# Performance work log

Measured on AMD Instinct MI355X. Metric: run time of the kernel, lower is better.

The kernel has to match this reference:

```python
import jax, jax.numpy as jnp
import numpy as np

B, QL, L = 4, 1024, 2048          # batch, new query tokens, cache capacity
H, KVH, D = 16, 4, 128            # query heads, kv heads (GQA), head dim
G = H // KVH                      # query heads per kv head
SCALE = 1.0 / float(np.sqrt(D))
NEG = jnp.float32(-1e30)


def setup_inputs() -> dict:
    key = jax.random.key(0)
    ks = jax.random.split(key, 6)
    return {
        "q": jax.random.normal(ks[0], (B, QL, H * D), jnp.float32),
        "k": jax.random.normal(ks[1], (B, QL, KVH * D), jnp.float32),
        "v": jax.random.normal(ks[2], (B, QL, KVH * D), jnp.float32),
        "cache_k": jax.random.normal(ks[3], (B, KVH, L, D), jnp.float32),
        "cache_v": jax.random.normal(ks[4], (B, KVH, L, D), jnp.float32),
        "seq_lens": jax.random.randint(ks[5], (B,), 0, L - QL, jnp.int32),
    }


def reference(q, k, v, cache_k, cache_v, seq_lens):
    bs, ql, _ = q.shape
    # split heads; scale applied to q as in _jax_attn_func
    qh = (q.reshape(bs, ql, H, D) * SCALE).swapaxes(1, 2)   # [B,H,QL,D]
    kh = k.reshape(bs, ql, KVH, D)                           # [B,QL,KVH,D]
    vh = v.reshape(bs, ql, KVH, D)
    # write new tokens into the kv cache at per-sequence positions (ragged)
    pos = seq_lens[:, None] + jnp.arange(ql)                 # [B,QL]
    bidx = jnp.arange(bs)[:, None]                           # [B,1]
    new_ck = cache_k.at[bidx, :, pos].set(kh)                # [B,KVH,L,D]
    new_cv = cache_v.at[bidx, :, pos].set(vh)
    # GQA attention over the full cache with ragged-causal mask
    qg = qh.reshape(bs, KVH, G, ql, D)                       # [B,KVH,G,QL,D]
    scores = jnp.einsum('bkgqd,bkld->bkgql', qg, new_ck)     # [B,KVH,G,QL,L]
    limit = seq_lens[:, None, None, None, None] + jnp.arange(ql)[None, None, None, :, None]
    valid = jnp.arange(L)[None, None, None, None, :] <= limit
    scores = jnp.where(valid, scores, NEG)
    probs = jax.nn.softmax(scores, axis=-1)
    outg = jnp.einsum('bkgql,bkld->bkgqd', probs, new_cv)    # [B,KVH,G,QL,D]
    out = outg.reshape(bs, H, ql, D).swapaxes(1, 2).reshape(bs, ql, H * D)
    return (out, new_ck, new_cv)
```

## Files before the change

kernel.cpp:

```cpp
#include <hip/hip_runtime.h>
#include <hip/hip_bf16.h>
#include <stdint.h>

#define NB 4
#define NQL 1024
#define NL 2048
#define NH 16
#define NKVH 4
#define ND 128
#define KVBLK 64
#define QSCALE_LOG2E 0.1275174340213733f

typedef __bf16 bf16_t;
typedef __bf16 bf16x4 __attribute__((ext_vector_type(4)));
typedef __bf16 bf16x8 __attribute__((ext_vector_type(8)));
typedef float f32x4 __attribute__((ext_vector_type(4)));
typedef float f32x16 __attribute__((ext_vector_type(16)));
typedef uint32_t u32;
typedef unsigned short u16;

__device__ __forceinline__ void gload_lds16(const void* g, void* l) {
  __builtin_amdgcn_global_load_lds((const __attribute__((address_space(1))) void*)g,
                                   (__attribute__((address_space(3))) void*)l,
                                   16, 0, 0);
}

__device__ __forceinline__ u32 pack_bf16(float a, float b) {
  u32 ua = (u32)__builtin_bit_cast(u16, (bf16_t)a);
  u32 ub = (u32)__builtin_bit_cast(u16, (bf16_t)b);
  return ua | (ub << 16);
}

__global__ __launch_bounds__(256) void update_cache_kernel(
    const float* __restrict__ knew,
    const float* __restrict__ vnew,
    const float* __restrict__ cache_k,
    const float* __restrict__ cache_v,
    const int*   __restrict__ seq_lens,
    float* __restrict__ new_ck,
    float* __restrict__ new_cv,
    bf16_t* __restrict__ kb)
{
  const int n4 = NB * NKVH * NL * ND / 4;
  for (int i = blockIdx.x * blockDim.x + threadIdx.x; i < 2 * n4;
       i += gridDim.x * blockDim.x) {
    const int which = i >= n4;
    const int j   = which ? i - n4 : i;
    const int d4  = j & 31;
    const int l   = (j >> 5) & (NL - 1);
    const int kvh = (j >> 16) & (NKVH - 1);
    const int b   = j >> 18;
    const int s   = seq_lens[b];
    float4 val;
    if (l >= s && l < s + NQL) {
      const float* nsrc = which ? vnew : knew;
      val = *(const float4*)(nsrc + (((size_t)(b * NQL + (l - s))) * NKVH + kvh) * ND + d4 * 4);
    } else {
      const float* csrc = which ? cache_v : cache_k;
      val = *(const float4*)(csrc + (((size_t)(b * NKVH + kvh)) * NL + l) * ND + d4 * 4);
    }
    const size_t coff = (((size_t)(b * NKVH + kvh)) * NL + l) * ND + d4 * 4;
    float* dst = which ? new_cv : new_ck;
    *(float4*)(dst + coff) = val;
    if (!which) {
      bf16x4 kv;
      kv[0] = (bf16_t)val.x; kv[1] = (bf16_t)val.y;
      kv[2] = (bf16_t)val.z; kv[3] = (bf16_t)val.w;
      *(bf16x4*)(kb + coff) = kv;
    }
  }
}

__global__ __launch_bounds__(256) void transpose_v_kernel(
    const float* __restrict__ new_cv, bf16_t* __restrict__ vt)
{
  __shared__ float T[64][129];
  const int tid = threadIdx.x;
  const int bid = blockIdx.x;
  const int lt  = bid & 31;
  const int kvh = (bid >> 5) & (NKVH - 1);
  const int b   = bid >> 7;
  const int l0  = lt * 64;

  const float* src = new_cv + (((size_t)(b * NKVH + kvh)) * NL + l0) * ND;
  #pragma unroll
  for (int j = 0; j < 8; ++j) {
    const int i   = tid + j * 256;
    const int row = i >> 5, c4 = i & 31;
    float4 v = *(const float4*)(src + row * ND + c4 * 4);
    T[row][c4 * 4 + 0] = v.x; T[row][c4 * 4 + 1] = v.y;
    T[row][c4 * 4 + 2] = v.z; T[row][c4 * 4 + 3] = v.w;
  }
  __syncthreads();
  bf16_t* dst = vt + ((size_t)(b * NKVH + kvh)) * ND * NL;
  #pragma unroll
  for (int j = 0; j < 4; ++j) {
    const int c = tid + j * 256;
    const int d = c >> 3, l8 = c & 7;
    bf16x8 o;
    #pragma unroll
    for (int e = 0; e < 8; ++e) o[e] = (bf16_t)T[l8 * 8 + e][d];
    *(bf16x8*)(dst + (size_t)d * NL + l0 + l8 * 8) = o;
  }
}

#define STAGE_K(buf, tt) do {                                                \
    const int l0s = (tt) * KVBLK;                                            \
    _Pragma("unroll")                                                        \
    for (int j = 0; j < 4; ++j) {                                            \
      const int ck = tid + j * 256;                                          \
      const int kr = ck >> 4, kc2 = (ck & 15) ^ (kr & 7);                    \
      gload_lds16(kbb + (size_t)(l0s + kr) * ND + kc2 * 8,                   \
                  &Kl[buf][(wave * 64 + j * 256) * 8]);                      \
    }                                                                        \
  } while (0)

#define STAGE_V(buf, tt) do {                                                \
    const int l0s = (tt) * KVBLK;                                            \
    _Pragma("unroll")                                                        \
    for (int j = 0; j < 4; ++j) {                                            \
      const int ck = tid + j * 256;                                          \
      const int vr = ck >> 3, vc2 = (ck & 7) ^ (vr & 7);                     \
      gload_lds16(vtb + (size_t)vr * NL + (l0s + vc2 * 8),                   \
                  &Vl[buf][(wave * 64 + j * 256) * 8]);                      \
    }                                                                        \
  } while (0)

#define QKT(SB, KBI) do {                                                    \
    _Pragma("unroll")                                                        \
    for (int sl = 0; sl < 2; ++sl) {                                         \
      f32x16 acc = (f32x16)(0.f);                                            \
      const int krow = sl * 32 + l5;                                         \
      _Pragma("unroll")                                                      \
      for (int kc = 0; kc < 8; ++kc) {                                       \
        bf16x8 kf = *(const bf16x8*)                                         \
            &Kl[KBI][krow * ND + (((kc * 2 + hi5) ^ (l5 & 7)) * 8)];         \
        acc = __builtin_amdgcn_mfma_f32_32x32x16_bf16(kf, qf[kc], acc, 0, 0, 0); \
      }                                                                      \
      SB[sl] = acc;                                                          \
    }                                                                        \
  } while (0)

#define SOFTPV(SB, VBI, L0) do {                                             \
    if ((L0) + 63 > s + qw) {                                                \
      const int lim = s + q - (L0);                                          \
      _Pragma("unroll")                                                      \
      for (int sl = 0; sl < 2; ++sl)                                         \
        _Pragma("unroll")                                                    \
        for (int rr = 0; rr < 16; ++rr) {                                    \
          const int ll = sl * 32 + (rr & 3) + 8 * (rr >> 2) + 4 * hi5;       \
          if (ll > lim) SB[sl][rr] = -1e30f;                                 \
        }                                                                    \
    }                                                                        \
    float pmax = SB[0][0];                                                   \
    _Pragma("unroll")                                                        \
    for (int sl = 0; sl < 2; ++sl)                                           \
      _Pragma("unroll")                                                      \
      for (int rr = 0; rr < 16; ++rr) pmax = fmaxf(pmax, SB[sl][rr]);        \
    pmax = fmaxf(pmax, __shfl_xor(pmax, 32, 64));                            \
    if (!__all(pmax - mreg <= 8.f)) {                                        \
      const float mnew  = fmaxf(mreg, pmax);                                 \
      const float alpha = exp2f(mreg - mnew);                                \
      mreg = mnew;                                                           \
      lreg *= alpha;                                                         \
      _Pragma("unroll")                                                      \
      for (int i = 0; i < 4; ++i) oacc[i] *= alpha;                          \
    }                                                                        \
    float tsum = 0.f;                                                        \
    _Pragma("unroll")                                                        \
    for (int sl = 0; sl < 2; ++sl)                                           \
      _Pragma("unroll")                                                      \
      for (int rr = 0; rr < 16; ++rr) {                                      \
        const float p = exp2f(SB[sl][rr] - mreg);                            \
        SB[sl][rr] = p;                                                      \
        tsum += p;                                                           \
      }                                                                      \
    lreg += tsum + __shfl_xor(tsum, 32, 64);                                 \
    u32 pk[2][4][2];                                                         \
    _Pragma("unroll")                                                        \
    for (int sl = 0; sl < 2; ++sl)                                           \
      _Pragma("unroll")                                                      \
      for (int m = 0; m < 4; ++m) {                                          \
        pk[sl][m][0] = pack_bf16(SB[sl][m * 4 + 0], SB[sl][m * 4 + 1]);      \
        pk[sl][m][1] = pack_bf16(SB[sl][m * 4 + 2], SB[sl][m * 4 + 3]);      \
      }                                                                      \
    bf16x8 pb[4];                                                            \
    _Pragma("unroll")                                                        \
    for (int c = 0; c < 4; ++c) {                                            \
      const int slp = c >> 1;                                                \
      const u32 k0 = hi5 ? pk[slp][(2 * c + 1) & 3][0] : pk[slp][(2 * c) & 3][0]; \
      const u32 k1 = hi5 ? pk[slp][(2 * c + 1) & 3][1] : pk[slp][(2 * c) & 3][1]; \
      const u32 s0 = hi5 ? pk[slp][(2 * c) & 3][0] : pk[slp][(2 * c + 1) & 3][0]; \
      const u32 s1 = hi5 ? pk[slp][(2 * c) & 3][1] : pk[slp][(2 * c + 1) & 3][1]; \
      const u32 r0 = (u32)__shfl_xor((int)s0, 32, 64);                       \
      const u32 r1 = (u32)__shfl_xor((int)s1, 32, 64);                       \
      union { u32 w[4]; bf16x8 v; } u;                                       \
      u.w[0] = hi5 ? r0 : k0;                                                \
      u.w[1] = hi5 ? r1 : k1;                                                \
      u.w[2] = hi5 ? k0 : r0;                                                \
      u.w[3] = hi5 ? k1 : r1;                                                \
      pb[c] = u.v;                                                           \
    }                                                                        \
    _Pragma("unroll")                                                        \
    for (int ds = 0; ds < 4; ++ds) {                                         \
      const int vrow = ds * 32 + l5;                                         \
      _Pragma("unroll")                                                      \
      for (int c = 0; c < 4; ++c) {                                          \
        bf16x8 va = *(const bf16x8*)                                         \
            &Vl[VBI][vrow * KVBLK + (((c * 2 + hi5) ^ (l5 & 7)) * 8)];       \
        oacc[ds] = __builtin_amdgcn_mfma_f32_32x32x16_bf16(va, pb[c], oacc[ds], 0, 0, 0); \
      }                                                                      \
    }                                                                        \
  } while (0)

__global__ __launch_bounds__(256, 2) void attn_kernel(
    const float* __restrict__ qin, const bf16_t* __restrict__ kb,
    const bf16_t* __restrict__ vt, const int* __restrict__ seq_lens,
    float* __restrict__ out)
{
  __shared__ bf16_t Kl[2][KVBLK * ND];
  __shared__ bf16_t Vl[2][ND * KVBLK];

  const int tid  = threadIdx.x;
  const int wave = tid >> 6, lane = tid & 63;
  const int l5   = lane & 31;
  const int hi5  = lane >> 5;

  const int bid  = blockIdx.x;
  const int half = bid >> 8, r = bid & 255;
  const int b    = r >> 6;
  const int h    = (r >> 2) & (NH - 1);
  const int qt   = half ? (7 - ((r & 3) << 1)) : ((r & 3) << 1);
  const int kvh  = h >> 2;
  const int s    = seq_lens[b];
  const int qw   = qt * 128 + wave * 32;
  const int q    = qw + l5;

  const bf16_t* kbb = kb + ((size_t)(b * NKVH + kvh)) * NL * ND;
  const bf16_t* vtb = vt + ((size_t)(b * NKVH + kvh)) * ND * NL;

  bf16x8 qf[8];
  {
    const float* qb = qin + ((size_t)((b * NQL + q) * NH + h)) * ND;
    #pragma unroll
    for (int kc = 0; kc < 8; ++kc) {
      float4 x0 = *(const float4*)(qb + kc * 16 + hi5 * 8);
      float4 x1 = *(const float4*)(qb + kc * 16 + hi5 * 8 + 4);
      bf16x8 f;
      f[0] = (bf16_t)(x0.x * QSCALE_LOG2E); f[1] = (bf16_t)(x0.y * QSCALE_LOG2E);
      f[2] = (bf16_t)(x0.z * QSCALE_LOG2E); f[3] = (bf16_t)(x0.w * QSCALE_LOG2E);
      f[4] = (bf16_t)(x1.x * QSCALE_LOG2E); f[5] = (bf16_t)(x1.y * QSCALE_LOG2E);
      f[6] = (bf16_t)(x1.z * QSCALE_LOG2E); f[7] = (bf16_t)(x1.w * QSCALE_LOG2E);
      qf[kc] = f;
    }
  }

  f32x16 oacc[4];
  #pragma unroll
  for (int i = 0; i < 4; ++i) oacc[i] = (f32x16)(0.f);
  float mreg = -1e30f, lreg = 0.f;

  const int ntiles = (s + qt * 128 + 128 + KVBLK - 1) / KVBLK;

  STAGE_K(0, 0);
  STAGE_V(0, 0);
  STAGE_K(1, 1);
  __syncthreads();

  f32x16 sA[2], sB[2];
  QKT(sA, 0);

  for (int t = 0; ; t += 2) {
    __syncthreads();
    if (t + 2 < ntiles) STAGE_K(0, t + 2);
    if (t + 1 < ntiles) STAGE_V(1, t + 1);
    const bool gB = (t + 1 < ntiles) && ((t + 1) * KVBLK <= s + qw + 31);
    if (gB) QKT(sB, 1);
    if (t * KVBLK <= s + qw + 31) SOFTPV(sA, 0, t * KVBLK);
    if (t + 1 >= ntiles) break;

    __syncthreads();
    if (t + 3 < ntiles) STAGE_K(1, t + 3);
    if (t + 2 < ntiles) STAGE_V(0, t + 2);
    const bool gA = (t + 2 < ntiles) && ((t + 2) * KVBLK <= s + qw + 31);
    if (gA) QKT(sA, 0);
    if ((t + 1) * KVBLK <= s + qw + 31) SOFTPV(sB, 1, (t + 1) * KVBLK);
    if (t + 2 >= ntiles) break;
  }

  const float linv = 1.0f / lreg;
  float* ob = out + ((size_t)((b * NQL + q) * NH + h)) * ND;
  #pragma unroll
  for (int ds = 0; ds < 4; ++ds)
    #pragma unroll
    for (int rq = 0; rq < 4; ++rq) {
      float4 v;
      v.x = oacc[ds][rq * 4 + 0] * linv;
      v.y = oacc[ds][rq * 4 + 1] * linv;
      v.z = oacc[ds][rq * 4 + 2] * linv;
      v.w = oacc[ds][rq * 4 + 3] * linv;
      *(float4*)(ob + ds * 32 + rq * 8 + hi5 * 4) = v;
    }
}

extern "C" void kernel_launch(void* const* d_in, const int* in_sizes, int n_in,
                              void* d_out, int out_size, void* d_ws, size_t ws_size,
                              hipStream_t stream)
{
  const float* q        = (const float*)d_in[0];
  const float* k        = (const float*)d_in[1];
  const float* v        = (const float*)d_in[2];
  const float* cache_k  = (const float*)d_in[3];
  const float* cache_v  = (const float*)d_in[4];
  const int*   seq_lens = (const int*)d_in[5];

  float* out    = (float*)d_out;
  float* new_ck = out + (size_t)NB * NQL * NH * ND;
  float* new_cv = new_ck + (size_t)NB * NKVH * NL * ND;

  bf16_t* kb = (bf16_t*)d_ws;
  bf16_t* vt = kb + (size_t)NB * NKVH * NL * ND;

  hipLaunchKernelGGL(update_cache_kernel, dim3(2048), dim3(256), 0, stream,
                     k, v, cache_k, cache_v, seq_lens, new_ck, new_cv, kb);
  hipLaunchKernelGGL(transpose_v_kernel, dim3(NB * NKVH * (NL / 64)), dim3(256), 0, stream,
                     new_cv, vt);
  hipLaunchKernelGGL(attn_kernel, dim3(512), dim3(256), 0, stream,
                     q, kb, vt, seq_lens, out);
}
```

Before: 110.2 us.

## Switch attention to 16x16x32 MFMA with smaller query and KV tiles

Reworks the attention kernel to use 16x16x32 bf16 MFMA instead of 32x32x16. Each wave now handles 16 query rows, KV tiles shrink to 32 rows, and the grid grows from 512 to 1024 blocks with occupancy raised to 4 blocks per CU. The P-matrix relayout now uses shuffles suited to the 16x16 fragment layout, and the causal-load-balancing block ordering is dropped. The aim is more parallelism and finer causal skipping, at the cost of more synchronisation per KV element, less data reuse per tile, and more shuffle overhead.

Measured after the change: 131.9 us. +19.7%, slower.

```diff
diff --git a/kernel.cpp b/kernel.cpp
--- a/kernel.cpp
+++ b/kernel.cpp
@@ -8,14 +8,13 @@
 #define NH 16
 #define NKVH 4
 #define ND 128
-#define KVBLK 64
+#define KVBLK 32
 #define QSCALE_LOG2E 0.1275174340213733f
 
 typedef __bf16 bf16_t;
 typedef __bf16 bf16x4 __attribute__((ext_vector_type(4)));
 typedef __bf16 bf16x8 __attribute__((ext_vector_type(8)));
 typedef float f32x4 __attribute__((ext_vector_type(4)));
-typedef float f32x16 __attribute__((ext_vector_type(16)));
 typedef uint32_t u32;
 typedef unsigned short u16;
 
@@ -107,7 +106,7 @@
 #define STAGE_K(buf, tt) do {                                                \
     const int l0s = (tt) * KVBLK;                                            \
     _Pragma("unroll")                                                        \
-    for (int j = 0; j < 4; ++j) {                                            \
+    for (int j = 0; j < 2; ++j) {                                            \
       const int ck = tid + j * 256;                                          \
       const int kr = ck >> 4, kc2 = (ck & 15) ^ (kr & 7);                    \
       gload_lds16(kbb + (size_t)(l0s + kr) * ND + kc2 * 8,                   \
@@ -118,9 +117,9 @@
 #define STAGE_V(buf, tt) do {                                                \
     const int l0s = (tt) * KVBLK;                                            \
     _Pragma("unroll")                                                        \
-    for (int j = 0; j < 4; ++j) {                                            \
+    for (int j = 0; j < 2; ++j) {                                            \
       const int ck = tid + j * 256;                                          \
-      const int vr = ck >> 3, vc2 = (ck & 7) ^ (vr & 7);                     \
+      const int vr = ck >> 2, vc2 = (ck & 3) ^ (vr & 3);                     \
       gload_lds16(vtb + (size_t)vr * NL + (l0s + vc2 * 8),                   \
                   &Vl[buf][(wave * 64 + j * 256) * 8]);                      \
     }                                                                        \
@@ -129,91 +128,72 @@
 #define QKT(SB, KBI) do {                                                    \
     _Pragma("unroll")                                                        \
     for (int sl = 0; sl < 2; ++sl) {                                         \
-      f32x16 acc = (f32x16)(0.f);                                            \
-      const int krow = sl * 32 + l5;                                         \
+      f32x4 acc = (f32x4){0.f, 0.f, 0.f, 0.f};                               \
       _Pragma("unroll")                                                      \
-      for (int kc = 0; kc < 8; ++kc) {                                       \
+      for (int kc = 0; kc < 4; ++kc) {                                       \
         bf16x8 kf = *(const bf16x8*)                                         \
-            &Kl[KBI][krow * ND + (((kc * 2 + hi5) ^ (l5 & 7)) * 8)];         \
-        acc = __builtin_amdgcn_mfma_f32_32x32x16_bf16(kf, qf[kc], acc, 0, 0, 0); \
+            &Kl[KBI][((sl * 16 + llo) * 16 + ((kc * 4 + lhi) ^ (llo & 7))) * 8]; \
+        acc = __builtin_amdgcn_mfma_f32_16x16x32_bf16(kf, qf[kc], acc, 0, 0, 0); \
       }                                                                      \
       SB[sl] = acc;                                                          \
     }                                                                        \
   } while (0)
 
 #define SOFTPV(SB, VBI, L0) do {                                             \
-    if ((L0) + 63 > s + qw) {                                                \
+    if ((L0) + 31 > s + qw) {                                                \
       const int lim = s + q - (L0);                                          \
       _Pragma("unroll")                                                      \
       for (int sl = 0; sl < 2; ++sl)                                         \
         _Pragma("unroll")                                                    \
-        for (int rr = 0; rr < 16; ++rr) {                                    \
-          const int ll = sl * 32 + (rr & 3) + 8 * (rr >> 2) + 4 * hi5;       \
-          if (ll > lim) SB[sl][rr] = -1e30f;                                 \
-        }                                                                    \
-    }                                                                        \
-    float pmax = SB[0][0];                                                   \
-    _Pragma("unroll")                                                        \
-    for (int sl = 0; sl < 2; ++sl)                                           \
-      _Pragma("unroll")                                                      \
-      for (int rr = 0; rr < 16; ++rr) pmax = fmaxf(pmax, SB[sl][rr]);        \
-    pmax = fmaxf(pmax, __shfl_xor(pmax, 32, 64));                            \
-    if (!__all(pmax - mreg <= 8.f)) {                                        \
-      const float mnew  = fmaxf(mreg, pmax);                                 \
+        for (int rr = 0; rr < 4; ++rr)                                       \
+          if (sl * 16 + lhi * 4 + rr > lim) SB[sl][rr] = -1e30f;             \
+    }                                                                        \
+    float pm = fmaxf(fmaxf(fmaxf(SB[0][0], SB[0][1]), fmaxf(SB[0][2], SB[0][3])), \
+                     fmaxf(fmaxf(SB[1][0], SB[1][1]), fmaxf(SB[1][2], SB[1][3]))); \
+    pm = fmaxf(pm, __shfl_xor(pm, 16, 64));                                  \
+    pm = fmaxf(pm, __shfl_xor(pm, 32, 64));                                  \
+    if (!__all(pm - mreg <= 8.f)) {                                          \
+      const float mnew  = fmaxf(mreg, pm);                                   \
       const float alpha = exp2f(mreg - mnew);                                \
       mreg = mnew;                                                           \
       lreg *= alpha;                                                         \
       _Pragma("unroll")                                                      \
-      for (int i = 0; i < 4; ++i) oacc[i] *= alpha;                          \
-    }                                                                        \
-    float tsum = 0.f;                                                        \
+      for (int i = 0; i < 8; ++i) oacc[i] *= alpha;                          \
+    }                                                                        \
+    const float p0 = exp2f(SB[0][0] - mreg), p1 = exp2f(SB[0][1] - mreg);    \
+    const float p2 = exp2f(SB[0][2] - mreg), p3 = exp2f(SB[0][3] - mreg);    \
+    const float p4 = exp2f(SB[1][0] - mreg), p5 = exp2f(SB[1][1] - mreg);    \
+    const float p6 = exp2f(SB[1][2] - mreg), p7 = exp2f(SB[1][3] - mreg);    \
+    float ts = ((p0 + p1) + (p2 + p3)) + ((p4 + p5) + (p6 + p7));            \
+    ts += __shfl_xor(ts, 16, 64);                                            \
+    ts += __shfl_xor(ts, 32, 64);                                            \
+    lreg += ts;                                                              \
+    const u32 pk00 = pack_bf16(p0, p1), pk01 = pack_bf16(p2, p3);            \
+    const u32 pk10 = pack_bf16(p4, p5), pk11 = pack_bf16(p6, p7);            \
+    const int src0 = ((lhi & 1) << 5) + llo;                                 \
+    const int src1 = src0 + 16;                                              \
+    const u32 a00 = (u32)__shfl((int)pk00, src0, 64);                        \
+    const u32 a01 = (u32)__shfl((int)pk01, src0, 64);                        \
+    const u32 a02 = (u32)__shfl((int)pk00, src1, 64);                        \
+    const u32 a03 = (u32)__shfl((int)pk01, src1, 64);                        \
+    const u32 a10 = (u32)__shfl((int)pk10, src0, 64);                        \
+    const u32 a11 = (u32)__shfl((int)pk11, src0, 64);                        \
+    const u32 a12 = (u32)__shfl((int)pk10, src1, 64);                        \
+    const u32 a13 = (u32)__shfl((int)pk11, src1, 64);                        \
+    union { u32 w[4]; bf16x8 v; } uu;                                        \
+    uu.w[0] = (lhi < 2) ? a00 : a10;                                         \
+    uu.w[1] = (lhi < 2) ? a01 : a11;                                         \
+    uu.w[2] = (lhi < 2) ? a02 : a12;                                         \
+    uu.w[3] = (lhi < 2) ? a03 : a13;                                         \
     _Pragma("unroll")                                                        \
-    for (int sl = 0; sl < 2; ++sl)                                           \
-      _Pragma("unroll")                                                      \
-      for (int rr = 0; rr < 16; ++rr) {                                      \
-        const float p = exp2f(SB[sl][rr] - mreg);                            \
-        SB[sl][rr] = p;                                                      \
-        tsum += p;                                                           \
-      }                                                                      \
-    lreg += tsum + __shfl_xor(tsum, 32, 64);                                 \
-    u32 pk[2][4][2];                                                         \
-    _Pragma("unroll")                                                        \
-    for (int sl = 0; sl < 2; ++sl)                                           \
-      _Pragma("unroll")                                                      \
-      for (int m = 0; m < 4; ++m) {                                          \
-        pk[sl][m][0] = pack_bf16(SB[sl][m * 4 + 0], SB[sl][m * 4 + 1]);      \
-        pk[sl][m][1] = pack_bf16(SB[sl][m * 4 + 2], SB[sl][m * 4 + 3]);      \
-      }                                                                      \
-    bf16x8 pb[4];                                                            \
-    _Pragma("unroll")                                                        \
-    for (int c = 0; c < 4; ++c) {                                            \
-      const int slp = c >> 1;                                                \
-      const u32 k0 = hi5 ? pk[slp][(2 * c + 1) & 3][0] : pk[slp][(2 * c) & 3][0]; \
-      const u32 k1 = hi5 ? pk[slp][(2 * c + 1) & 3][1] : pk[slp][(2 * c) & 3][1]; \
-      const u32 s0 = hi5 ? pk[slp][(2 * c) & 3][0] : pk[slp][(2 * c + 1) & 3][0]; \
-      const u32 s1 = hi5 ? pk[slp][(2 * c) & 3][1] : pk[slp][(2 * c + 1) & 3][1]; \
-      const u32 r0 = (u32)__shfl_xor((int)s0, 32, 64);                       \
-      const u32 r1 = (u32)__shfl_xor((int)s1, 32, 64);                       \
-      union { u32 w[4]; bf16x8 v; } u;                                       \
-      u.w[0] = hi5 ? r0 : k0;                                                \
-      u.w[1] = hi5 ? r1 : k1;                                                \
-      u.w[2] = hi5 ? k0 : r0;                                                \
-      u.w[3] = hi5 ? k1 : r1;                                                \
-      pb[c] = u.v;                                                           \
-    }                                                                        \
-    _Pragma("unroll")                                                        \
-    for (int ds = 0; ds < 4; ++ds) {                                         \
-      const int vrow = ds * 32 + l5;                                         \
-      _Pragma("unroll")                                                      \
-      for (int c = 0; c < 4; ++c) {                                          \
-        bf16x8 va = *(const bf16x8*)                                         \
-            &Vl[VBI][vrow * KVBLK + (((c * 2 + hi5) ^ (l5 & 7)) * 8)];       \
-        oacc[ds] = __builtin_amdgcn_mfma_f32_32x32x16_bf16(va, pb[c], oacc[ds], 0, 0, 0); \
-      }                                                                      \
+    for (int dsb = 0; dsb < 8; ++dsb) {                                      \
+      bf16x8 va = *(const bf16x8*)                                           \
+          &Vl[VBI][((dsb * 16 + llo) * 4 + (lhi ^ (llo & 3))) * 8];          \
+      oacc[dsb] = __builtin_amdgcn_mfma_f32_16x16x32_bf16(va, uu.v, oacc[dsb], 0, 0, 0); \
     }                                                                        \
   } while (0)
 
-__global__ __launch_bounds__(256, 2) void attn_kernel(
+__global__ __launch_bounds__(256, 4) void attn_kernel(
     const float* __restrict__ qin, const bf16_t* __restrict__ kb,
     const bf16_t* __restrict__ vt, const int* __restrict__ seq_lens,
     float* __restrict__ out)
@@ -223,29 +203,29 @@
 
   const int tid  = threadIdx.x;
   const int wave = tid >> 6, lane = tid & 63;
-  const int l5   = lane & 31;
-  const int hi5  = lane >> 5;
-
-  const int bid  = blockIdx.x;
-  const int half = bid >> 8, r = bid & 255;
-  const int b    = r >> 6;
-  const int h    = (r >> 2) & (NH - 1);
-  const int qt   = half ? (7 - ((r & 3) << 1)) : ((r & 3) << 1);
-  const int kvh  = h >> 2;
-  const int s    = seq_lens[b];
-  const int qw   = qt * 128 + wave * 32;
-  const int q    = qw + l5;
+  const int llo  = lane & 15;
+  const int lhi  = lane >> 4;
+
+  const int bid = blockIdx.x;
+  const int b   = bid >> 8;
+  const int r   = bid & 255;
+  const int h   = r >> 4;
+  const int qt  = r & 15;
+  const int kvh = h >> 2;
+  const int s   = seq_lens[b];
+  const int qw  = qt * 64 + wave * 16;
+  const int q   = qw + llo;
 
   const bf16_t* kbb = kb + ((size_t)(b * NKVH + kvh)) * NL * ND;
   const bf16_t* vtb = vt + ((size_t)(b * NKVH + kvh)) * ND * NL;
 
-  bf16x8 qf[8];
+  bf16x8 qf[4];
   {
     const float* qb = qin + ((size_t)((b * NQL + q) * NH + h)) * ND;
     #pragma unroll
-    for (int kc = 0; kc < 8; ++kc) {
-      float4 x0 = *(const float4*)(qb + kc * 16 + hi5 * 8);
-      float4 x1 = *(const float4*)(qb + kc * 16 + hi5 * 8 + 4);
+    for (int kc = 0; kc < 4; ++kc) {
+      float4 x0 = *(const float4*)(qb + kc * 32 + lhi * 8);
+      float4 x1 = *(const float4*)(qb + kc * 32 + lhi * 8 + 4);
       bf16x8 f;
       f[0] = (bf16_t)(x0.x * QSCALE_LOG2E); f[1] = (bf16_t)(x0.y * QSCALE_LOG2E);
       f[2] = (bf16_t)(x0.z * QSCALE_LOG2E); f[3] = (bf16_t)(x0.w * QSCALE_LOG2E);
@@ -255,52 +235,50 @@
     }
   }
 
-  f32x16 oacc[4];
+  f32x4 oacc[8];
   #pragma unroll
-  for (int i = 0; i < 4; ++i) oacc[i] = (f32x16)(0.f);
+  for (int i = 0; i < 8; ++i) oacc[i] = (f32x4){0.f, 0.f, 0.f, 0.f};
   float mreg = -1e30f, lreg = 0.f;
 
-  const int ntiles = (s + qt * 128 + 128 + KVBLK - 1) / KVBLK;
+  const int ntiles = (s + qt * 64 + 64 + KVBLK - 1) / KVBLK;
 
   STAGE_K(0, 0);
   STAGE_V(0, 0);
   STAGE_K(1, 1);
   __syncthreads();
 
-  f32x16 sA[2], sB[2];
+  f32x4 sA[2], sB[2];
   QKT(sA, 0);
 
   for (int t = 0; ; t += 2) {
     __syncthreads();
     if (t + 2 < ntiles) STAGE_K(0, t + 2);
     if (t + 1 < ntiles) STAGE_V(1, t + 1);
-    const bool gB = (t + 1 < ntiles) && ((t + 1) * KVBLK <= s + qw + 31);
+    const bool gB = (t + 1 < ntiles) && ((t + 1) * KVBLK <= s + qw + 15);
     if (gB) QKT(sB, 1);
-    if (t * KVBLK <= s + qw + 31) SOFTPV(sA, 0, t * KVBLK);
+    if (t * KVBLK <= s + qw + 15) SOFTPV(sA, 0, t * KVBLK);
     if (t + 1 >= ntiles) break;
 
     __syncthreads();
     if (t + 3 < ntiles) STAGE_K(1, t + 3);
     if (t + 2 < ntiles) STAGE_V(0, t + 2);
-    const bool gA = (t + 2 < ntiles) && ((t + 2) * KVBLK <= s + qw + 31);
+    const bool gA = (t + 2 < ntiles) && ((t + 2) * KVBLK <= s + qw + 15);
     if (gA) QKT(sA, 0);
-    if ((t + 1) * KVBLK <= s + qw + 31) SOFTPV(sB, 1, (t + 1) * KVBLK);
+    if ((t + 1) * KVBLK <= s + qw + 15) SOFTPV(sB, 1, (t + 1) * KVBLK);
     if (t + 2 >= ntiles) break;
   }
 
   const float linv = 1.0f / lreg;
   float* ob = out + ((size_t)((b * NQL + q) * NH + h)) * ND;
   #pragma unroll
-  for (int ds = 0; ds < 4; ++ds)
-    #pragma unroll
-    for (int rq = 0; rq < 4; ++rq) {
-      float4 v;
-      v.x = oacc[ds][rq * 4 + 0] * linv;
-      v.y = oacc[ds][rq * 4 + 1] * linv;
-      v.z = oacc[ds][rq * 4 + 2] * linv;
-      v.w = oacc[ds][rq * 4 + 3] * linv;
-      *(float4*)(ob + ds * 32 + rq * 8 + hi5 * 4) = v;
-    }
+  for (int dsb = 0; dsb < 8; ++dsb) {
+    float4 v;
+    v.x = oacc[dsb][0] * linv;
+    v.y = oacc[dsb][1] * linv;
+    v.z = oacc[dsb][2] * linv;
+    v.w = oacc[dsb][3] * linv;
+    *(float4*)(ob + dsb * 16 + lhi * 4) = v;
+  }
 }
 
 extern "C" void kernel_launch(void* const* d_in, const int* in_sizes, int n_in,
@@ -325,6 +303,6 @@
                      k, v, cache_k, cache_v, seq_lens, new_ck, new_cv, kb);
   hipLaunchKernelGGL(transpose_v_kernel, dim3(NB * NKVH * (NL / 64)), dim3(256), 0, stream,
                      new_cv, vt);
-  hipLaunchKernelGGL(attn_kernel, dim3(512), dim3(256), 0, stream,
+  hipLaunchKernelGGL(attn_kernel, dim3(NB * NH * (NQL / 64)), dim3(256), 0, stream,
                      q, kb, vt, seq_lens, out);
 }
```

## Split KV range across two blocks with combine kernel and smaller KV tile

Applied to the files above, without the earlier changes.

Adds a split-KV (flash-decoding style) scheme: each (batch, kv head, q tile) is split into two KV ranges. Each range writes bf16 partial outputs plus running max and sum, and a new combine kernel merges them into the final output. The KV tile shrinks from 64 to 32 rows with a new V swizzle, and launch bounds rise to 4 blocks per SM to raise occupancy. The goal is more parallelism and better load balance across the causal triangle. The cost is an extra kernel launch, more global traffic for partials, and bf16 rounding of the partial accumulators.

New measurement: 262.7 us. 138% more time.

```diff
diff --git a/kernel.cpp b/kernel.cpp
--- a/kernel.cpp
+++ b/kernel.cpp
@@ -8,7 +8,8 @@
 #define NH 16
 #define NKVH 4
 #define ND 128
-#define KVBLK 64
+#define KVBLK 32
+#define NROWS (NB * NH * NQL)
 #define QSCALE_LOG2E 0.1275174340213733f
 
 typedef __bf16 bf16_t;
@@ -107,7 +108,7 @@
 #define STAGE_K(buf, tt) do {                                                \
     const int l0s = (tt) * KVBLK;                                            \
     _Pragma("unroll")                                                        \
-    for (int j = 0; j < 4; ++j) {                                            \
+    for (int j = 0; j < 2; ++j) {                                            \
       const int ck = tid + j * 256;                                          \
       const int kr = ck >> 4, kc2 = (ck & 15) ^ (kr & 7);                    \
       gload_lds16(kbb + (size_t)(l0s + kr) * ND + kc2 * 8,                   \
@@ -118,105 +119,93 @@
 #define STAGE_V(buf, tt) do {                                                \
     const int l0s = (tt) * KVBLK;                                            \
     _Pragma("unroll")                                                        \
-    for (int j = 0; j < 4; ++j) {                                            \
+    for (int j = 0; j < 2; ++j) {                                            \
       const int ck = tid + j * 256;                                          \
-      const int vr = ck >> 3, vc2 = (ck & 7) ^ (vr & 7);                     \
+      const int vr = ck >> 2, vc2 = (ck & 3) ^ ((vr ^ (vr >> 2)) & 3);       \
       gload_lds16(vtb + (size_t)vr * NL + (l0s + vc2 * 8),                   \
                   &Vl[buf][(wave * 64 + j * 256) * 8]);                      \
     }                                                                        \
   } while (0)
 
 #define QKT(SB, KBI) do {                                                    \
-    _Pragma("unroll")                                                        \
-    for (int sl = 0; sl < 2; ++sl) {                                         \
-      f32x16 acc = (f32x16)(0.f);                                            \
-      const int krow = sl * 32 + l5;                                         \
-      _Pragma("unroll")                                                      \
-      for (int kc = 0; kc < 8; ++kc) {                                       \
-        bf16x8 kf = *(const bf16x8*)                                         \
-            &Kl[KBI][krow * ND + (((kc * 2 + hi5) ^ (l5 & 7)) * 8)];         \
-        acc = __builtin_amdgcn_mfma_f32_32x32x16_bf16(kf, qf[kc], acc, 0, 0, 0); \
-      }                                                                      \
-      SB[sl] = acc;                                                          \
-    }                                                                        \
+    f32x16 acc = (f32x16)(0.f);                                              \
+    _Pragma("unroll")                                                        \
+    for (int kc = 0; kc < 8; ++kc) {                                         \
+      bf16x8 kf = *(const bf16x8*)                                           \
+          &Kl[KBI][(l5 * 16 + ((kc * 2 + hi5) ^ (l5 & 7))) * 8];             \
+      acc = __builtin_amdgcn_mfma_f32_32x32x16_bf16(kf, qf[kc], acc, 0, 0, 0); \
+    }                                                                        \
+    SB = acc;                                                                \
   } while (0)
 
 #define SOFTPV(SB, VBI, L0) do {                                             \
-    if ((L0) + 63 > s + qw) {                                                \
+    if ((L0) + 31 > s + qw) {                                                \
       const int lim = s + q - (L0);                                          \
       _Pragma("unroll")                                                      \
-      for (int sl = 0; sl < 2; ++sl)                                         \
-        _Pragma("unroll")                                                    \
-        for (int rr = 0; rr < 16; ++rr) {                                    \
-          const int ll = sl * 32 + (rr & 3) + 8 * (rr >> 2) + 4 * hi5;       \
-          if (ll > lim) SB[sl][rr] = -1e30f;                                 \
-        }                                                                    \
-    }                                                                        \
-    float pmax = SB[0][0];                                                   \
-    _Pragma("unroll")                                                        \
-    for (int sl = 0; sl < 2; ++sl)                                           \
-      _Pragma("unroll")                                                      \
-      for (int rr = 0; rr < 16; ++rr) pmax = fmaxf(pmax, SB[sl][rr]);        \
-    pmax = fmaxf(pmax, __shfl_xor(pmax, 32, 64));                            \
-    if (!__all(pmax - mreg <= 8.f)) {                                        \
-      const float mnew  = fmaxf(mreg, pmax);                                 \
+      for (int rr = 0; rr < 16; ++rr) {                                      \
+        const int ll = (rr & 3) + 8 * (rr >> 2) + 4 * hi5;                   \
+        if (ll > lim) SB[rr] = -1e30f;                                       \
+      }                                                                      \
+    }                                                                        \
+    float pm = SB[0];                                                        \
+    _Pragma("unroll")                                                        \
+    for (int rr = 1; rr < 16; ++rr) pm = fmaxf(pm, SB[rr]);                  \
+    pm = fmaxf(pm, __shfl_xor(pm, 32, 64));                                  \
+    if (!__all(pm - mreg <= 8.f)) {                                          \
+      const float mnew  = fmaxf(mreg, pm);                                   \
       const float alpha = exp2f(mreg - mnew);                                \
       mreg = mnew;                                                           \
       lreg *= alpha;                                                         \
       _Pragma("unroll")                                                      \
       for (int i = 0; i < 4; ++i) oacc[i] *= alpha;                          \
     }                                                                        \
-    float tsum = 0.f;                                                        \
-    _Pragma("unroll")                                                        \
-    for (int sl = 0; sl < 2; ++sl)                                           \
-      _Pragma("unroll")                                                      \
-      for (int rr = 0; rr < 16; ++rr) {                                      \
-        const float p = exp2f(SB[sl][rr] - mreg);                            \
-        SB[sl][rr] = p;                                                      \
-        tsum += p;                                                           \
-      }                                                                      \
-    lreg += tsum + __shfl_xor(tsum, 32, 64);                                 \
-    u32 pk[2][4][2];                                                         \
-    _Pragma("unroll")                                                        \
-    for (int sl = 0; sl < 2; ++sl)                                           \
-      _Pragma("unroll")                                                      \
-      for (int m = 0; m < 4; ++m) {                                          \
-        pk[sl][m][0] = pack_bf16(SB[sl][m * 4 + 0], SB[sl][m * 4 + 1]);      \
-        pk[sl][m][1] = pack_bf16(SB[sl][m * 4 + 2], SB[sl][m * 4 + 3]);      \
-      }                                                                      \
-    bf16x8 pb[4];                                                            \
-    _Pragma("unroll")                                                        \
-    for (int c = 0; c < 4; ++c) {                                            \
-      const int slp = c >> 1;                                                \
-      const u32 k0 = hi5 ? pk[slp][(2 * c + 1) & 3][0] : pk[slp][(2 * c) & 3][0]; \
-      const u32 k1 = hi5 ? pk[slp][(2 * c + 1) & 3][1] : pk[slp][(2 * c) & 3][1]; \
-      const u32 s0 = hi5 ? pk[slp][(2 * c) & 3][0] : pk[slp][(2 * c + 1) & 3][0]; \
-      const u32 s1 = hi5 ? pk[slp][(2 * c) & 3][1] : pk[slp][(2 * c + 1) & 3][1]; \
-      const u32 r0 = (u32)__shfl_xor((int)s0, 32, 64);                       \
-      const u32 r1 = (u32)__shfl_xor((int)s1, 32, 64);                       \
-      union { u32 w[4]; bf16x8 v; } u;                                       \
-      u.w[0] = hi5 ? r0 : k0;                                                \
-      u.w[1] = hi5 ? r1 : k1;                                                \
-      u.w[2] = hi5 ? k0 : r0;                                                \
-      u.w[3] = hi5 ? k1 : r1;                                                \
-      pb[c] = u.v;                                                           \
+    float ts = 0.f;                                                          \
+    _Pragma("unroll")                                                        \
+    for (int rr = 0; rr < 16; ++rr) {                                        \
+      const float p = exp2f(SB[rr] - mreg);                                  \
+      SB[rr] = p;                                                            \
+      ts += p;                                                               \
+    }                                                                        \
+    lreg += ts + __shfl_xor(ts, 32, 64);                                     \
+    u32 pk[4][2];                                                            \
+    _Pragma("unroll")                                                        \
+    for (int m = 0; m < 4; ++m) {                                            \
+      pk[m][0] = pack_bf16(SB[m * 4 + 0], SB[m * 4 + 1]);                    \
+      pk[m][1] = pack_bf16(SB[m * 4 + 2], SB[m * 4 + 3]);                    \
+    }                                                                        \
+    bf16x8 pb[2];                                                            \
+    _Pragma("unroll")                                                        \
+    for (int c = 0; c < 2; ++c) {                                            \
+      const u32 own0 = hi5 ? pk[c * 2 + 1][0] : pk[c * 2][0];                \
+      const u32 own1 = hi5 ? pk[c * 2 + 1][1] : pk[c * 2][1];                \
+      const u32 snd0 = hi5 ? pk[c * 2][0] : pk[c * 2 + 1][0];                \
+      const u32 snd1 = hi5 ? pk[c * 2][1] : pk[c * 2 + 1][1];                \
+      const u32 r0 = (u32)__shfl_xor((int)snd0, 32, 64);                     \
+      const u32 r1 = (u32)__shfl_xor((int)snd1, 32, 64);                     \
+      union { u32 w[4]; bf16x8 v; } uu;                                      \
+      uu.w[0] = hi5 ? r0 : own0;                                             \
+      uu.w[1] = hi5 ? r1 : own1;                                             \
+      uu.w[2] = hi5 ? own0 : r0;                                             \
+      uu.w[3] = hi5 ? own1 : r1;                                             \
+      pb[c] = uu.v;                                                          \
     }                                                                        \
     _Pragma("unroll")                                                        \
     for (int ds = 0; ds < 4; ++ds) {                                         \
       const int vrow = ds * 32 + l5;                                         \
       _Pragma("unroll")                                                      \
-      for (int c = 0; c < 4; ++c) {                                          \
+      for (int c = 0; c < 2; ++c) {                                          \
         bf16x8 va = *(const bf16x8*)                                         \
-            &Vl[VBI][vrow * KVBLK + (((c * 2 + hi5) ^ (l5 & 7)) * 8)];       \
+            &Vl[VBI][(vrow * 4 + ((c * 2 + hi5) ^ ((l5 ^ (l5 >> 2)) & 3))) * 8]; \
         oacc[ds] = __builtin_amdgcn_mfma_f32_32x32x16_bf16(va, pb[c], oacc[ds], 0, 0, 0); \
       }                                                                      \
     }                                                                        \
   } while (0)
 
-__global__ __launch_bounds__(256, 2) void attn_kernel(
+__global__ __launch_bounds__(256, 4) void attn_kernel(
     const float* __restrict__ qin, const bf16_t* __restrict__ kb,
     const bf16_t* __restrict__ vt, const int* __restrict__ seq_lens,
-    float* __restrict__ out)
+    float* __restrict__ out, bf16_t* __restrict__ opart,
+    float2* __restrict__ ml, int nspl)
 {
   __shared__ bf16_t Kl[2][KVBLK * ND];
   __shared__ bf16_t Vl[2][ND * KVBLK];
@@ -226,18 +215,21 @@
   const int l5   = lane & 31;
   const int hi5  = lane >> 5;
 
-  const int bid  = blockIdx.x;
-  const int half = bid >> 8, r = bid & 255;
-  const int b    = r >> 6;
-  const int h    = (r >> 2) & (NH - 1);
-  const int qt   = half ? (7 - ((r & 3) << 1)) : ((r & 3) << 1);
-  const int kvh  = h >> 2;
-  const int s    = seq_lens[b];
-  const int qw   = qt * 128 + wave * 32;
-  const int q    = qw + l5;
-
-  const bf16_t* kbb = kb + ((size_t)(b * NKVH + kvh)) * NL * ND;
-  const bf16_t* vtb = vt + ((size_t)(b * NKVH + kvh)) * ND * NL;
+  const int bid = blockIdx.x;
+  const int qt  = bid & 7;
+  const int hh  = (bid >> 3) & 3;
+  const int g   = bid >> 5;
+  const int sp  = g - (g / nspl) * nspl;
+  const int bk  = g / nspl;
+  const int kvh = bk & (NKVH - 1);
+  const int b   = bk >> 2;
+  const int h   = kvh * 4 + hh;
+  const int s   = seq_lens[b];
+  const int qw  = qt * 128 + wave * 32;
+  const int q   = qw + l5;
+
+  const bf16_t* kbb = kb + ((size_t)bk) * NL * ND;
+  const bf16_t* vtb = vt + ((size_t)bk) * ND * NL;
 
   bf16x8 qf[8];
   {
@@ -260,47 +252,90 @@
   for (int i = 0; i < 4; ++i) oacc[i] = (f32x16)(0.f);
   float mreg = -1e30f, lreg = 0.f;
 
-  const int ntiles = (s + qt * 128 + 128 + KVBLK - 1) / KVBLK;
-
-  STAGE_K(0, 0);
-  STAGE_V(0, 0);
-  STAGE_K(1, 1);
+  const int nt   = (s + qt * 128 + 128 + KVBLK - 1) / KVBLK;
+  const int half = (nt + nspl - 1) / nspl;
+  const int t0   = sp * half;
+  const int t1   = (sp + 1 == nspl) ? nt : (t0 + half);
+  const int vlim = s + qw + 31;
+
+  STAGE_K(0, t0);
+  STAGE_V(0, t0);
+  STAGE_K(1, t0 + 1);
   __syncthreads();
 
-  f32x16 sA[2], sB[2];
+  f32x16 sA, sB;
   QKT(sA, 0);
 
-  for (int t = 0; ; t += 2) {
+  for (int t = t0; ; t += 2) {
     __syncthreads();
-    if (t + 2 < ntiles) STAGE_K(0, t + 2);
-    if (t + 1 < ntiles) STAGE_V(1, t + 1);
-    const bool gB = (t + 1 < ntiles) && ((t + 1) * KVBLK <= s + qw + 31);
+    if (t + 2 < t1) STAGE_K(0, t + 2);
+    if (t + 1 < t1) STAGE_V(1, t + 1);
+    const bool gB = (t + 1 < t1) && ((t + 1) * KVBLK <= vlim);
     if (gB) QKT(sB, 1);
-    if (t * KVBLK <= s + qw + 31) SOFTPV(sA, 0, t * KVBLK);
-    if (t + 1 >= ntiles) break;
+    if (t * KVBLK <= vlim) SOFTPV(sA, 0, t * KVBLK);
+    if (t + 1 >= t1) break;
 
     __syncthreads();
-    if (t + 3 < ntiles) STAGE_K(1, t + 3);
-    if (t + 2 < ntiles) STAGE_V(0, t + 2);
-    const bool gA = (t + 2 < ntiles) && ((t + 2) * KVBLK <= s + qw + 31);
+    if (t + 3 < t1) STAGE_K(1, t + 3);
+    if (t + 2 < t1) STAGE_V(0, t + 2);
+    const bool gA = (t + 2 < t1) && ((t + 2) * KVBLK <= vlim);
     if (gA) QKT(sA, 0);
-    if ((t + 1) * KVBLK <= s + qw + 31) SOFTPV(sB, 1, (t + 1) * KVBLK);
-    if (t + 2 >= ntiles) break;
-  }
-
-  const float linv = 1.0f / lreg;
-  float* ob = out + ((size_t)((b * NQL + q) * NH + h)) * ND;
-  #pragma unroll
-  for (int ds = 0; ds < 4; ++ds)
+    if ((t + 1) * KVBLK <= vlim) SOFTPV(sB, 1, (t + 1) * KVBLK);
+    if (t + 2 >= t1) break;
+  }
+
+  const int row = (b * NH + h) * NQL + q;
+  if (nspl == 1) {
+    const float linv = 1.0f / lreg;
+    float* ob = out + ((size_t)((b * NQL + q) * NH + h)) * ND;
     #pragma unroll
-    for (int rq = 0; rq < 4; ++rq) {
-      float4 v;
-      v.x = oacc[ds][rq * 4 + 0] * linv;
-      v.y = oacc[ds][rq * 4 + 1] * linv;
-      v.z = oacc[ds][rq * 4 + 2] * linv;
-      v.w = oacc[ds][rq * 4 + 3] * linv;
-      *(float4*)(ob + ds * 32 + rq * 8 + hi5 * 4) = v;
-    }
+    for (int ds = 0; ds < 4; ++ds)
+      #pragma unroll
+      for (int rq = 0; rq < 4; ++rq) {
+        float4 v;
+        v.x = oacc[ds][rq * 4 + 0] * linv;
+        v.y = oacc[ds][rq * 4 + 1] * linv;
+        v.z = oacc[ds][rq * 4 + 2] * linv;
+        v.w = oacc[ds][rq * 4 + 3] * linv;
+        *(float4*)(ob + ds * 32 + rq * 8 + hi5 * 4) = v;
+      }
+  } else {
+    bf16_t* ob = opart + ((size_t)sp * NROWS + row) * ND;
+    #pragma unroll
+    for (int ds = 0; ds < 4; ++ds)
+      #pragma unroll
+      for (int rq = 0; rq < 4; ++rq) {
+        bf16x4 v;
+        v[0] = (bf16_t)oacc[ds][rq * 4 + 0];
+        v[1] = (bf16_t)oacc[ds][rq * 4 + 1];
+        v[2] = (bf16_t)oacc[ds][rq * 4 + 2];
+        v[3] = (bf16_t)oacc[ds][rq * 4 + 3];
+        *(bf16x4*)(ob + ds * 32 + rq * 8 + hi5 * 4) = v;
+      }
+    if (hi5 == 0) ml[(size_t)sp * NROWS + row] = make_float2(mreg, lreg);
+  }
+}
+
+__global__ __launch_bounds__(256) void combine_kernel(
+    const bf16_t* __restrict__ opart, const float2* __restrict__ ml,
+    float* __restrict__ out)
+{
+  const int gid = blockIdx.x * 256 + threadIdx.x;
+  const int row = gid >> 5, d4 = gid & 31;
+  const float2 ml0 = ml[row];
+  const float2 ml1 = ml[NROWS + row];
+  const float M  = fmaxf(ml0.x, ml1.x);
+  const float a0 = exp2f(ml0.x - M), a1 = exp2f(ml1.x - M);
+  const float linv = 1.0f / (a0 * ml0.y + a1 * ml1.y);
+  bf16x4 o0 = *(const bf16x4*)(opart + (size_t)row * ND + d4 * 4);
+  bf16x4 o1 = *(const bf16x4*)(opart + ((size_t)NROWS + row) * ND + d4 * 4);
+  const int q = row & (NQL - 1), h = (row >> 10) & (NH - 1), b = row >> 14;
+  float4 v;
+  v.x = (a0 * (float)o0[0] + a1 * (float)o1[0]) * linv;
+  v.y = (a0 * (float)o0[1] + a1 * (float)o1[1]) * linv;
+  v.z = (a0 * (float)o0[2] + a1 * (float)o1[2]) * linv;
+  v.w = (a0 * (float)o0[3] + a1 * (float)o1[3]) * linv;
+  *(float4*)(out + ((size_t)((b * NQL + q) * NH + h)) * ND + d4 * 4) = v;
 }
 
 extern "C" void kernel_launch(void* const* d_in, const int* in_sizes, int n_in,
@@ -318,13 +353,22 @@
   float* new_ck = out + (size_t)NB * NQL * NH * ND;
   float* new_cv = new_ck + (size_t)NB * NKVH * NL * ND;
 
-  bf16_t* kb = (bf16_t*)d_ws;
-  bf16_t* vt = kb + (size_t)NB * NKVH * NL * ND;
+  const size_t cache_elems = (size_t)NB * NKVH * NL * ND;
+  bf16_t* kb    = (bf16_t*)d_ws;
+  bf16_t* vt    = kb + cache_elems;
+  bf16_t* opart = vt + cache_elems;
+  float2* ml    = (float2*)(opart + (size_t)2 * NROWS * ND);
+
+  const size_t need = (size_t)((char*)(ml + 2 * NROWS) - (char*)d_ws);
+  const int nspl = (ws_size >= need) ? 2 : 1;
 
   hipLaunchKernelGGL(update_cache_kernel, dim3(2048), dim3(256), 0, stream,
                      k, v, cache_k, cache_v, seq_lens, new_ck, new_cv, kb);
   hipLaunchKernelGGL(transpose_v_kernel, dim3(NB * NKVH * (NL / 64)), dim3(256), 0, stream,
                      new_cv, vt);
-  hipLaunchKernelGGL(attn_kernel, dim3(512), dim3(256), 0, stream,
-                     q, kb, vt, seq_lens, out);
-}
+  hipLaunchKernelGGL(attn_kernel, dim3(NB * NKVH * nspl * 32), dim3(256), 0, stream,
+                     q, kb, vt, seq_lens, out, opart, ml, nspl);
+  if (nspl == 2)
+    hipLaunchKernelGGL(combine_kernel, dim3(NROWS * 32 / 256), dim3(256), 0, stream,
+                       opart, ml, out);
+}
```
